# Kernel optimization log

Measured on AMD Instinct MI355X. Metric: run time of the kernel, lower is better.

The kernel has to match this reference:

```python
import jax, jax.numpy as jnp
import numpy as np

N, E, F_IN, C, H = 50000, 800000, 256, 64, 2  # nodes, edges, in-feat, per-head dim, heads
NEG_SLOPE_ATT = 0.2   # GATConv leaky_relu slope
NEG_SLOPE = 0.01      # F.leaky_relu default
BN_EPS = 1e-5


def setup_inputs() -> dict:
    key = jax.random.key(0)
    ks = jax.random.split(key, 10)
    x = jax.random.normal(ks[0], (N, F_IN), dtype=jnp.float32)
    edge_index = jax.random.randint(ks[1], (2, E), 0, N, dtype=jnp.int32)
    # GATConv params
    W = jax.random.normal(ks[2], (F_IN, H * C), dtype=jnp.float32) / np.sqrt(F_IN)
    att_src = jax.random.normal(ks[3], (H, C), dtype=jnp.float32) / np.sqrt(C)
    att_dst = jax.random.normal(ks[4], (H, C), dtype=jnp.float32) / np.sqrt(C)
    conv_bias = jnp.zeros((H * C,), dtype=jnp.float32)
    # fc1: in = hidden*2*2 = 256, out = hidden = 64
    fc1_w = jax.random.normal(ks[5], (H * C * 2, C), dtype=jnp.float32) / np.sqrt(H * C * 2)
    fc1_b = jnp.zeros((C,), dtype=jnp.float32)
    bn_gamma = jnp.ones((C,), dtype=jnp.float32)
    bn_beta = jnp.zeros((C,), dtype=jnp.float32)
    bn_mean = jnp.zeros((C,), dtype=jnp.float32)
    bn_var = jnp.ones((C,), dtype=jnp.float32)
    fc2_w = jax.random.normal(ks[6], (C, 3), dtype=jnp.float32) / np.sqrt(C)
    fc2_b = jnp.zeros((3,), dtype=jnp.float32)
    return {"x": x, "edge_index": edge_index, "W": W, "att_src": att_src,
            "att_dst": att_dst, "conv_bias": conv_bias, "fc1_w": fc1_w, "fc1_b": fc1_b,
            "bn_gamma": bn_gamma, "bn_beta": bn_beta, "bn_mean": bn_mean,
            "bn_var": bn_var, "fc2_w": fc2_w, "fc2_b": fc2_b}


def gat_conv(x, edge_index, W, att_src, att_dst, bias):
    # Project: [N, H, C]
    h = (x @ W).reshape(N, H, C)
    a_s = jnp.einsum('nhc,hc->nh', h, att_src)  # [N, H]
    a_d = jnp.einsum('nhc,hc->nh', h, att_dst)
    # add self-loops (PyG default)
    loops = jnp.arange(N, dtype=edge_index.dtype)
    src = jnp.concatenate([edge_index[0], loops])
    dst = jnp.concatenate([edge_index[1], loops])
    e = jax.nn.leaky_relu(a_s[src] + a_d[dst], NEG_SLOPE_ATT)  # [E+N, H]
    # segment softmax over incoming edges of each dst node
    m = jax.ops.segment_max(e, dst, num_segments=N)
    e_exp = jnp.exp(e - m[dst])
    denom = jax.ops.segment_sum(e_exp, dst, num_segments=N)
    alpha = e_exp / denom[dst]  # [E+N, H]
    msg = h[src] * alpha[:, :, None]  # [E+N, H, C]
    out = jax.ops.segment_sum(msg, dst, num_segments=N)  # [N, H, C]
    return out.reshape(N, H * C) + bias


def reference(x, edge_index, W, att_src, att_dst, conv_bias, fc1_w, fc1_b,
              bn_gamma, bn_beta, bn_mean, bn_var, fc2_w, fc2_b):
    # eval mode: dropout = identity, BN uses running stats
    h = gat_conv(x, edge_index, W, att_src, att_dst, conv_bias)
    h = jax.nn.leaky_relu(h, NEG_SLOPE)
    edge_rep = jnp.concatenate([h[edge_index[0]], h[edge_index[1]]], axis=1)  # [E, 256]
    y = edge_rep @ fc1_w + fc1_b
    y = (y - bn_mean) * jax.lax.rsqrt(bn_var + BN_EPS) * bn_gamma + bn_beta
    y = jax.nn.leaky_relu(y, NEG_SLOPE)
    return y @ fc2_w + fc2_b  # [E, 3]
```

## Files before the change

### kernel.cpp

```cpp
#include <hip/hip_runtime.h>
#include <hip/hip_bf16.h>

#define N_NODES 50000
#define N_EDGES 800000
#define F_IN    256
#define C_DIM   64
#define HC      128
#define NPG     6250
#define NBB     32
#define NBLK    196
#define XW_BLOCKS   3125
#define HIST_BLOCKS 256

typedef __attribute__((ext_vector_type(8))) short bf16x8;
typedef __attribute__((ext_vector_type(4))) float f32x4;

static constexpr size_t OFF_HBF   = 0;
static constexpr size_t OFF_AB    = 25600000;
static constexpr size_t OFF_AS    = 38400000;
static constexpr size_t OFF_AD    = 38800000;
static constexpr size_t OFF_OFFS  = 39200000;
static constexpr size_t OFF_TOT   = 39400064;
static constexpr size_t OFF_PART  = 39800064;
static constexpr size_t OFF_CSR2  = 39801088;
static constexpr size_t OFF_WT    = 46201088;
static constexpr size_t OFF_FC1T  = 46266624;
static constexpr size_t OFF_SCALE = 46299392;
static constexpr size_t OFF_CC    = 46299904;
static constexpr size_t OFF_FC2M  = 46300416;
static constexpr size_t OFF_BCNT  = 46302464;
static constexpr size_t OFF_BASE  = 52702464;

__device__ __forceinline__ float2 bf2(unsigned u) {
    float2 r;
    r.x = __uint_as_float(u << 16);
    r.y = __uint_as_float(u & 0xffff0000u);
    return r;
}
__device__ __forceinline__ unsigned short f2bf(float f) {
    unsigned u = __float_as_uint(f);
    return (unsigned short)((u + 0x7fffu + ((u >> 16) & 1u)) >> 16);
}
__device__ __forceinline__ short f2bf_s(float f) {
    __hip_bfloat16 h = __float2bfloat16(f);
    return *reinterpret_cast<short*>(&h);
}

__global__ __launch_bounds__(256) void k_prep(const float* __restrict__ W,
                                              const float* __restrict__ fc1,
                                              const float* __restrict__ fc1_b,
                                              const float* __restrict__ gamma,
                                              const float* __restrict__ beta,
                                              const float* __restrict__ mean,
                                              const float* __restrict__ var,
                                              const float* __restrict__ fc2_w,
                                              unsigned short* __restrict__ Wt,
                                              unsigned short* __restrict__ fc1t,
                                              float* __restrict__ scale,
                                              float* __restrict__ cc,
                                              unsigned short* __restrict__ fc2m) {
    int id = blockIdx.x * 256 + threadIdx.x;
    if (id < 32768) {
        int n = id >> 8, k = id & 255;
        Wt[id] = f2bf(W[k * HC + n]);
    }
    int id2 = id - 32768;
    if (id2 >= 0 && id2 < 16384) {
        int j = id2 >> 7, q = id2 & 127;
        int L = q >> 1, b = q & 1;
        int kch = 32 * (L >> 4) + (L & 15) + 16 * b;
        float v = (j < 64) ? fc1[kch * 64 + j] : fc1[(128 + kch) * 64 + (j - 64)];
        fc1t[id2] = f2bf(v);
    }
    int id3 = id - (32768 + 16384);
    if (id3 >= 0 && id3 < 128) {
        int jj = id3 & 63;
        float s = gamma[jj] * rsqrtf(var[jj] + 1e-5f);
        scale[id3] = s;
        cc[id3] = (id3 < 64) ? 0.f : (fc1_b[jj] - mean[jj]) * s + beta[jj];
    }
    int id4 = id - (32768 + 16384 + 128);
    if (id4 >= 0 && id4 < 1024) {
        int kk = id4 >> 9, rem = id4 & 511;
        int lane = rem >> 3, j = rem & 7;
        int q  = kk * 16 + (lane >> 4) * 4 + (j >> 1);
        int ch = 32 * (q >> 4) + (q & 15) + 16 * (j & 1);
        int col = lane & 15;
        float v = (col < 3) ? fc2_w[ch * 3 + col] : 0.f;
        fc2m[id4] = f2bf(v);
    }
}

__global__ __launch_bounds__(256, 4) void k_front(const float* __restrict__ x,
                                                  const unsigned short* __restrict__ Wt,
                                                  const float* __restrict__ att_src,
                                                  const float* __restrict__ att_dst,
                                                  unsigned* __restrict__ h_p,
                                                  float* __restrict__ as_,
                                                  float* __restrict__ ad_,
                                                  const int* __restrict__ dst,
                                                  int* __restrict__ bcnt) {
    __shared__ int smem[6464];
    const int t = threadIdx.x;

    if (blockIdx.x < HIST_BLOCKS) {
        int* hist = smem;
        const int bid = blockIdx.x;
        const int g  = bid & 7;
        const int bi = bid >> 3;
        const int lo = g * NPG, hi = lo + NPG;
        for (int j = t; j < NPG; j += 256) hist[j] = 0;
        __syncthreads();
        const int4* d4 = (const int4*)dst + bi * 6250;
#pragma unroll 1
        for (int it = 0; it < 25; ++it) {
            int idx = it * 256 + t;
            if (idx < 6250) {
                int4 d = d4[idx];
                if (d.x >= lo && d.x < hi) atomicAdd(&hist[d.x - lo], 1);
                if (d.y >= lo && d.y < hi) atomicAdd(&hist[d.y - lo], 1);
                if (d.z >= lo && d.z < hi) atomicAdd(&hist[d.z - lo], 1);
                if (d.w >= lo && d.w < hi) atomicAdd(&hist[d.w - lo], 1);
            }
        }
        __syncthreads();
        int* row = bcnt + (size_t)(g * NBB + bi) * NPG;
        for (int j = t; j < NPG; j += 256) row[j] = hist[j];
        return;
    }

    float* xs  = (float*)smem;
    float* sAs = (float*)(smem + 4096);
    float* sAd = sAs + 32;
    const int v    = t >> 6;
    const int lane = t & 63;
    const int c16  = lane & 15;
    const int kg   = lane >> 4;
    const int r0   = (blockIdx.x - HIST_BLOCKS) * 16;
    if (t < 32) { sAs[t] = 0.f; sAd[t] = 0.f; }
    {
        const float4* xsrc = (const float4*)(x + (size_t)r0 * F_IN);
        float4* xsl = (float4*)xs;
#pragma unroll
        for (int it = 0; it < 4; ++it) {
            int cidx = it * 256 + t;
            int rl = cidx >> 6, j = cidx & 63;
            float4 val = xsrc[cidx];
            xsl[rl * 64 + (j ^ rl)] = val;
        }
    }
    const int cf0 = 2 * v, cf1 = 2 * v + 1;
    bf16x8 wf0[8], wf1[8];
#pragma unroll
    for (int kk = 0; kk < 8; ++kk) {
        wf0[kk] = *(const bf16x8*)(Wt + (size_t)(cf0 * 16 + c16) * 256 + kk * 32 + kg * 8);
        wf1[kk] = *(const bf16x8*)(Wt + (size_t)(cf1 * 16 + c16) * 256 + kk * 32 + kg * 8);
    }
    __syncthreads();

    f32x4 acc0 = {}, acc1 = {};
#pragma unroll
    for (int kk = 0; kk < 8; ++kk) {
        int j0 = kk * 8 + kg * 2;
        float4 a0 = *(const float4*)(xs + (size_t)(c16 * 64 + (j0 ^ c16)) * 4);
        float4 a1 = *(const float4*)(xs + (size_t)(c16 * 64 + ((j0 + 1) ^ c16)) * 4);
        float fv[8] = {a0.x, a0.y, a0.z, a0.w, a1.x, a1.y, a1.z, a1.w};
        bf16x8 ahi, alo;
#pragma unroll
        for (int q = 0; q < 8; ++q) {
            unsigned u = __float_as_uint(fv[q]);
            float hval = __uint_as_float(u & 0xffff0000u);
            float d = fv[q] - hval;
            ahi[q] = (short)(u >> 16);
            alo[q] = (short)(__float_as_uint(d) >> 16);
        }
        acc0 = __builtin_amdgcn_mfma_f32_16x16x32_bf16(alo, wf0[kk], acc0, 0, 0, 0);
        acc0 = __builtin_amdgcn_mfma_f32_16x16x32_bf16(ahi, wf0[kk], acc0, 0, 0, 0);
        acc1 = __builtin_amdgcn_mfma_f32_16x16x32_bf16(alo, wf1[kk], acc1, 0, 0, 0);
        acc1 = __builtin_amdgcn_mfma_f32_16x16x32_bf16(ahi, wf1[kk], acc1, 0, 0, 0);
    }
#pragma unroll
    for (int i = 0; i < 4; ++i) {
        int row = r0 + kg * 4 + i;
        unsigned pu = (unsigned)f2bf(acc0[i]) | ((unsigned)f2bf(acc1[i]) << 16);
        h_p[(size_t)row * 64 + v * 16 + c16] = pu;
    }
    float ws0 = att_src[cf0 * 16 + c16], ws1 = att_src[cf1 * 16 + c16];
    float wd0 = att_dst[cf0 * 16 + c16], wd1 = att_dst[cf1 * 16 + c16];
    float pas[4], pad[4];
#pragma unroll
    for (int i = 0; i < 4; ++i) {
        pas[i] = acc0[i] * ws0 + acc1[i] * ws1;
        pad[i] = acc0[i] * wd0 + acc1[i] * wd1;
    }
#pragma unroll
    for (int m = 1; m < 16; m <<= 1) {
#pragma unroll
        for (int i = 0; i < 4; ++i) {
            pas[i] += __shfl_xor(pas[i], m, 64);
            pad[i] += __shfl_xor(pad[i], m, 64);
        }
    }
    const int head = v >> 1;
    if (c16 == 0) {
#pragma unroll
        for (int i = 0; i < 4; ++i) {
            atomicAdd(&sAs[(kg * 4 + i) * 2 + head], pas[i]);
            atomicAdd(&sAd[(kg * 4 + i) * 2 + head], pad[i]);
        }
    }
    __syncthreads();
    if (t < 32) {
        int row = t >> 1, hd = t & 1;
        as_[(r0 + row) * 2 + hd] = sAs[row * 2 + hd];
        ad_[(r0 + row) * 2 + hd] = sAd[row * 2 + hd];
    }
}

__global__ void k_tot_part(const int* __restrict__ bcnt, int* __restrict__ tot,
                           int* __restrict__ part) {
    __shared__ int sd[256];
    int n = blockIdx.x * 256 + threadIdx.x;
    int s = 0;
    if (n < N_NODES) {
        int g = n / NPG, ln = n - g * NPG;
        const int* col = bcnt + (size_t)g * NBB * NPG + ln;
#pragma unroll
        for (int bi = 0; bi < NBB; ++bi) s += col[bi * NPG];
        tot[n] = s;
    }
    sd[threadIdx.x] = s;
    __syncthreads();
    for (int off = 128; off > 0; off >>= 1) {
        if (threadIdx.x < off) sd[threadIdx.x] += sd[threadIdx.x + off];
        __syncthreads();
    }
    if (threadIdx.x == 0) part[blockIdx.x] = sd[0];
}

__global__ void k_scan_base(const int* __restrict__ tot, const int* __restrict__ part,
                            const int* __restrict__ bcnt, int* __restrict__ offs,
                            int* __restrict__ base) {
    __shared__ int sp[256];
    __shared__ int sd[256];
    const int t = threadIdx.x;
    int pv = (t < NBLK && t < (int)blockIdx.x) ? part[t] : 0;
    sp[t] = pv;
    __syncthreads();
    for (int off = 128; off > 0; off >>= 1) {
        if (t < off) sp[t] += sp[t + off];
        __syncthreads();
    }
    const int bb = sp[0];
    __syncthreads();
    int i = blockIdx.x * 256 + t;
    int v = (i < N_NODES) ? tot[i] : 0;
    sd[t] = v;
    __syncthreads();
    for (int off = 1; off < 256; off <<= 1) {
        int u = (t >= off) ? sd[t - off] : 0;
        __syncthreads();
        sd[t] += u;
        __syncthreads();
    }
    if (i < N_NODES) {
        int o = bb + sd[t] - v;
        offs[i] = o;
        if (i == N_NODES - 1) offs[N_NODES] = o + v;
        int g = i / NPG, ln = i - g * NPG;
        const int* col = bcnt + (size_t)g * NBB * NPG + ln;
        int* bcol = base + (size_t)g * NBB * NPG + ln;
        int run = o;
#pragma unroll
        for (int bi = 0; bi < NBB; ++bi) {
            bcol[bi * NPG] = run;
            run += col[bi * NPG];
        }
    }
}

__global__ __launch_bounds__(256) void k_scatter(const int* __restrict__ src,
                                                 const int* __restrict__ dst,
                                                 const int* __restrict__ base,
                                                 int2* __restrict__ csr2) {
    __shared__ int cnt[NPG];
    const int g  = blockIdx.x & 7;
    const int bi = blockIdx.x >> 3;
    const int lo = g * NPG, hi = lo + NPG;
    const int* brow = base + (size_t)(g * NBB + bi) * NPG;
    for (int j = threadIdx.x; j < NPG; j += 256) cnt[j] = brow[j];
    __syncthreads();
    const int4* d4 = (const int4*)dst + bi * 6250;
    const int4* s4 = (const int4*)src + bi * 6250;
    const int ebase = bi * 25000;
#pragma unroll 1
    for (int it = 0; it < 25; ++it) {
        int idx = it * 256 + threadIdx.x;
        if (idx < 6250) {
            int4 d = d4[idx];
            int4 s = s4[idx];
            int e = ebase + idx * 4;
            if (d.x >= lo && d.x < hi) { int p = atomicAdd(&cnt[d.x - lo], 1); csr2[p] = make_int2(s.x, e);     }
            if (d.y >= lo && d.y < hi) { int p = atomicAdd(&cnt[d.y - lo], 1); csr2[p] = make_int2(s.y, e + 1); }
            if (d.z >= lo && d.z < hi) { int p = atomicAdd(&cnt[d.z - lo], 1); csr2[p] = make_int2(s.z, e + 2); }
            if (d.w >= lo && d.w < hi) { int p = atomicAdd(&cnt[d.w - lo], 1); csr2[p] = make_int2(s.w, e + 3); }
        }
    }
}

__global__ __launch_bounds__(256) void k_agg_uv(const unsigned* __restrict__ h_p,
                                                const float* __restrict__ as_,
                                                const float* __restrict__ ad_,
                                                const int* __restrict__ offs,
                                                const int2* __restrict__ csr2,
                                                const float* __restrict__ conv_bias,
                                                const unsigned short* __restrict__ fc1t,
                                                const float* __restrict__ scale,
                                                const float* __restrict__ cc,
                                                unsigned* __restrict__ ab_p) {
    __shared__ unsigned lds_h2[16 * 68];
    const int t    = threadIdx.x;
    const int v    = t >> 6;
    const int lane = t & 63;
    const int ql   = lane & 15;
    const int q    = lane >> 4;
    const int hd   = ql >> 3;
    const int nbase = blockIdx.x * 16;
    const uint4* h4 = (const uint4*)h_p;

#pragma unroll 1
    for (int j = 0; j < 4; ++j) {
        const int ln = v * 4 + j;
        const int n  = nbase + ln;
        const float adn = ad_[n * 2 + hd];
        float a[8] = {};
        float accw = 0.f;
        const int beg = offs[n], end = offs[n + 1];
        int i = beg + q;
        for (; i + 4 < end; i += 8) {
            int s0 = csr2[i].x;
            int s1 = csr2[i + 4].x;
            uint4 u0 = h4[(unsigned)(s0 * 16 + ql)];
            uint4 u1 = h4[(unsigned)(s1 * 16 + ql)];
            float l0 = as_[s0 * 2 + hd] + adn;
            float l1 = as_[s1 * 2 + hd] + adn;
            l0 = fmaxf(l0, 0.2f * l0);
            l1 = fmaxf(l1, 0.2f * l1);
            float w0 = __expf(l0), w1 = __expf(l1);
            float2 tt;
            tt = bf2(u0.x); a[0] += w0 * tt.x; a[1] += w0 * tt.y;
            tt = bf2(u0.y); a[2] += w0 * tt.x; a[3] += w0 * tt.y;
            tt = bf2(u0.z); a[4] += w0 * tt.x; a[5] += w0 * tt.y;
            tt = bf2(u0.w); a[6] += w0 * tt.x; a[7] += w0 * tt.y;
            tt = bf2(u1.x); a[0] += w1 * tt.x; a[1] += w1 * tt.y;
            tt = bf2(u1.y); a[2] += w1 * tt.x; a[3] += w1 * tt.y;
            tt = bf2(u1.z); a[4] += w1 * tt.x; a[5] += w1 * tt.y;
            tt = bf2(u1.w); a[6] += w1 * tt.x; a[7] += w1 * tt.y;
            accw += w0 + w1;
        }
        if (i < end) {
            int s0 = csr2[i].x;
            uint4 u0 = h4[(unsigned)(s0 * 16 + ql)];
            float l0 = as_[s0 * 2 + hd] + adn;
            l0 = fmaxf(l0, 0.2f * l0);
            float w0 = __expf(l0);
            float2 tt;
            tt = bf2(u0.x); a[0] += w0 * tt.x; a[1] += w0 * tt.y;
            tt = bf2(u0.y); a[2] += w0 * tt.x; a[3] += w0 * tt.y;
            tt = bf2(u0.z); a[4] += w0 * tt.x; a[5] += w0 * tt.y;
            tt = bf2(u0.w); a[6] += w0 * tt.x; a[7] += w0 * tt.y;
            accw += w0;
        }
#pragma unroll
        for (int m = 16; m < 64; m <<= 1) {
#pragma unroll
            for (int jj = 0; jj < 8; ++jj) a[jj] += __shfl_xor(a[jj], m, 64);
            accw += __shfl_xor(accw, m, 64);
        }
        if (q == 0) {
            float es = as_[n * 2 + hd] + adn;
            es = fmaxf(es, 0.2f * es);
            float wsl = __expf(es);
            uint4 un = h4[(unsigned)(n * 16 + ql)];
            float2 tt;
            tt = bf2(un.x); a[0] += wsl * tt.x; a[1] += wsl * tt.y;
            tt = bf2(un.y); a[2] += wsl * tt.x; a[3] += wsl * tt.y;
            tt = bf2(un.z); a[4] += wsl * tt.x; a[5] += wsl * tt.y;
            tt = bf2(un.w); a[6] += wsl * tt.x; a[7] += wsl * tt.y;
            accw += wsl;
            float rinv = 1.f / accw;
            unsigned pw[4];
#pragma unroll
            for (int jj = 0; jj < 4; ++jj) {
                int w = 4 * ql + jj;
                int c = 32 * (w >> 4) + (w & 15);
                float o0 = a[2 * jj] * rinv + conv_bias[c];
                float o1 = a[2 * jj + 1] * rinv + conv_bias[c + 16];
                o0 = fmaxf(o0, 0.01f * o0);
                o1 = fmaxf(o1, 0.01f * o1);
                pw[jj] = (unsigned)f2bf(o0) | ((unsigned)f2bf(o1) << 16);
            }
            *(uint4*)&lds_h2[ln * 68 + ql * 4] = make_uint4(pw[0], pw[1], pw[2], pw[3]);
        }
    }
    __syncthreads();

    const int c16 = lane & 15;
    const int kg  = lane >> 4;
    const int cf0 = 2 * v, cf1 = 2 * v + 1;
    bf16x8 af[4];
#pragma unroll
    for (int kk = 0; kk < 4; ++kk)
        af[kk] = *(const bf16x8*)&lds_h2[c16 * 68 + kk * 16 + kg * 4];
    f32x4 acc0 = {}, acc1 = {};
#pragma unroll
    for (int kk = 0; kk < 4; ++kk) {
        bf16x8 b0 = *(const bf16x8*)(fc1t + (size_t)(cf0 * 16 + c16) * HC + kk * 32 + kg * 8);
        bf16x8 b1 = *(const bf16x8*)(fc1t + (size_t)(cf1 * 16 + c16) * HC + kk * 32 + kg * 8);
        acc0 = __builtin_amdgcn_mfma_f32_16x16x32_bf16(af[kk], b0, acc0, 0, 0, 0);
        acc1 = __builtin_amdgcn_mfma_f32_16x16x32_bf16(af[kk], b1, acc1, 0, 0, 0);
    }
    const int j0 = cf0 * 16 + c16, j1 = j0 + 16;
    const float s0 = scale[j0], s1 = scale[j1];
    const float q0 = cc[j0],    q1 = cc[j1];
#pragma unroll
    for (int i = 0; i < 4; ++i) {
        int row = nbase + kg * 4 + i;
        unsigned pu = (unsigned)f2bf(acc0[i] * s0 + q0)
                    | ((unsigned)f2bf(acc1[i] * s1 + q1) << 16);
        ab_p[(size_t)row * 64 + v * 16 + c16] = pu;
    }
}

__device__ __forceinline__ void mk_afrag(uint4 ua, const float* bb, bf16x8& ap) {
    float2 t; float z;
    t = bf2(ua.x);
    z = t.x + bb[0]; z = fmaxf(z, 0.01f * z); ap[0] = f2bf_s(z);
    z = t.y + bb[1]; z = fmaxf(z, 0.01f * z); ap[1] = f2bf_s(z);
    t = bf2(ua.y);
    z = t.x + bb[2]; z = fmaxf(z, 0.01f * z); ap[2] = f2bf_s(z);
    z = t.y + bb[3]; z = fmaxf(z, 0.01f * z); ap[3] = f2bf_s(z);
    t = bf2(ua.z);
    z = t.x + bb[4]; z = fmaxf(z, 0.01f * z); ap[4] = f2bf_s(z);
    z = t.y + bb[5]; z = fmaxf(z, 0.01f * z); ap[5] = f2bf_s(z);
    t = bf2(ua.w);
    z = t.x + bb[6]; z = fmaxf(z, 0.01f * z); ap[6] = f2bf_s(z);
    z = t.y + bb[7]; z = fmaxf(z, 0.01f * z); ap[7] = f2bf_s(z);
}

__global__ __launch_bounds__(256) void k_edge(const int* __restrict__ offs,
                                              const int2* __restrict__ csr2,
                                              const unsigned* __restrict__ ab_p,
                                              const unsigned short* __restrict__ fc2m,
                                              const float* __restrict__ fc2_b,
                                              float* __restrict__ out) {
    const int n    = blockIdx.x * 4 + (threadIdx.x >> 6);
    const int lane = threadIdx.x & 63;
    const int c16  = lane & 15;
    const int kg   = lane >> 4;
    bf16x8 bfr0 = *(const bf16x8*)(fc2m + (size_t)lane * 8);
    bf16x8 bfr1 = *(const bf16x8*)(fc2m + (size_t)(64 + lane) * 8);
    const uint4* abv = (const uint4*)ab_p;
    uint4 ub0 = abv[(unsigned)(n * 16 + 8 + kg)];
    uint4 ub1 = abv[(unsigned)(n * 16 + 12 + kg)];
    float bb0[8], bb1[8];
    {
        float2 t;
        t = bf2(ub0.x); bb0[0] = t.x; bb0[1] = t.y;
        t = bf2(ub0.y); bb0[2] = t.x; bb0[3] = t.y;
        t = bf2(ub0.z); bb0[4] = t.x; bb0[5] = t.y;
        t = bf2(ub0.w); bb0[6] = t.x; bb0[7] = t.y;
        t = bf2(ub1.x); bb1[0] = t.x; bb1[1] = t.y;
        t = bf2(ub1.y); bb1[2] = t.x; bb1[3] = t.y;
        t = bf2(ub1.z); bb1[4] = t.x; bb1[5] = t.y;
        t = bf2(ub1.w); bb1[6] = t.x; bb1[7] = t.y;
    }
    const float ob = (c16 < 3) ? fc2_b[c16] : 0.f;
    const int beg = offs[n], end = offs[n + 1];
    for (int base = beg; base < end; base += 16) {
        int slot = base + c16;
        int2 ce = (slot < end) ? csr2[slot] : make_int2(0, 0);
        uint4 ua0 = abv[(unsigned)(ce.x * 16 + kg)];
        uint4 ua1 = abv[(unsigned)(ce.x * 16 + 4 + kg)];
        bf16x8 ap0, ap1;
        mk_afrag(ua0, bb0, ap0);
        mk_afrag(ua1, bb1, ap1);
        f32x4 acc = {};
        acc = __builtin_amdgcn_mfma_f32_16x16x32_bf16(ap0, bfr0, acc, 0, 0, 0);
        acc = __builtin_amdgcn_mfma_f32_16x16x32_bf16(ap1, bfr1, acc, 0, 0, 0);
#pragma unroll
        for (int i = 0; i < 4; ++i) {
            int eid = __shfl(ce.y, kg * 4 + i, 64);
            if (c16 < 3 && (base + kg * 4 + i) < end)
                out[(size_t)eid * 3 + c16] = acc[i] + ob;
        }
    }
}

extern "C" void kernel_launch(void* const* d_in, const int* in_sizes, int n_in,
                              void* d_out, int out_size, void* d_ws, size_t ws_size,
                              hipStream_t stream) {
    const float* x        = (const float*)d_in[0];
    const int*   ei       = (const int*)d_in[1];
    const float* W        = (const float*)d_in[2];
    const float* att_src  = (const float*)d_in[3];
    const float* att_dst  = (const float*)d_in[4];
    const float* conv_b   = (const float*)d_in[5];
    const float* fc1_w    = (const float*)d_in[6];
    const float* fc1_b    = (const float*)d_in[7];
    const float* gamma    = (const float*)d_in[8];
    const float* beta     = (const float*)d_in[9];
    const float* mean     = (const float*)d_in[10];
    const float* var      = (const float*)d_in[11];
    const float* fc2_w    = (const float*)d_in[12];
    const float* fc2_b    = (const float*)d_in[13];
    float*       out      = (float*)d_out;
    char*        ws       = (char*)d_ws;

    const int* src = ei;
    const int* dst = ei + N_EDGES;

    unsigned*       h_p   = (unsigned*)(ws + OFF_HBF);
    unsigned*       ab_p  = (unsigned*)(ws + OFF_AB);
    float*          as_   = (float*)(ws + OFF_AS);
    float*          ad_   = (float*)(ws + OFF_AD);
    int*            offs  = (int*)(ws + OFF_OFFS);
    int*            tot   = (int*)(ws + OFF_TOT);
    int*            part  = (int*)(ws + OFF_PART);
    int2*           csr2  = (int2*)(ws + OFF_CSR2);
    unsigned short* Wt    = (unsigned short*)(ws + OFF_WT);
    unsigned short* fc1t  = (unsigned short*)(ws + OFF_FC1T);
    float*          scale = (float*)(ws + OFF_SCALE);
    float*          cc    = (float*)(ws + OFF_CC);
    unsigned short* fc2m  = (unsigned short*)(ws + OFF_FC2M);
    int*            bcnt  = (int*)(ws + OFF_BCNT);
    int*            base  = (int*)(ws + OFF_BASE);

    k_prep<<<235, 256, 0, stream>>>(W, fc1_w, fc1_b, gamma, beta, mean, var, fc2_w,
                                    Wt, fc1t, scale, cc, fc2m);

    k_front<<<HIST_BLOCKS + XW_BLOCKS, 256, 0, stream>>>(x, Wt, att_src, att_dst,
                                                         h_p, as_, ad_, dst, bcnt);

    k_tot_part <<<NBLK, 256, 0, stream>>>(bcnt, tot, part);
    k_scan_base<<<NBLK, 256, 0, stream>>>(tot, part, bcnt, offs, base);
    k_scatter  <<<8 * NBB, 256, 0, stream>>>(src, dst, base, csr2);

    k_agg_uv<<<N_NODES / 16, 256, 0, stream>>>(h_p, as_, ad_, offs, csr2, conv_b,
                                               fc1t, scale, cc, ab_p);
    k_edge  <<<N_NODES / 4, 256, 0, stream>>>(offs, csr2, ab_p, fc2m, fc2_b, out);
}
```

Baseline: 151.6 us.

## Process edges in original order in edge kernel and shrink CSR to source-only

The edge MLP kernel now walks edges in their original order, one 16-edge tile per wave, instead of walking each destination node's CSR segment. Each tile gathers both the source and destination precomputed halves, and its output rows are written contiguously rather than scattered through stored edge ids. The CSR therefore only needs source indices, which halves the scatter writes and the aggregation reads. The cost is an extra random gather of the destination half per edge (previously loaded once per node). It also removes per-node loop imbalance and partially empty tiles.

```diff
diff --git a/kernel.cpp b/kernel.cpp
--- a/kernel.cpp
+++ b/kernel.cpp
@@ -22,7 +22,7 @@
 static constexpr size_t OFF_OFFS  = 39200000;
 static constexpr size_t OFF_TOT   = 39400064;
 static constexpr size_t OFF_PART  = 39800064;
-static constexpr size_t OFF_CSR2  = 39801088;
+static constexpr size_t OFF_CSR   = 39801088;
 static constexpr size_t OFF_WT    = 46201088;
 static constexpr size_t OFF_FC1T  = 46266624;
 static constexpr size_t OFF_SCALE = 46299392;
@@ -282,7 +282,7 @@
 __global__ __launch_bounds__(256) void k_scatter(const int* __restrict__ src,
                                                  const int* __restrict__ dst,
                                                  const int* __restrict__ base,
-                                                 int2* __restrict__ csr2) {
+                                                 int* __restrict__ csr) {
     __shared__ int cnt[NPG];
     const int g  = blockIdx.x & 7;
     const int bi = blockIdx.x >> 3;
@@ -292,18 +292,16 @@
     __syncthreads();
     const int4* d4 = (const int4*)dst + bi * 6250;
     const int4* s4 = (const int4*)src + bi * 6250;
-    const int ebase = bi * 25000;
 #pragma unroll 1
     for (int it = 0; it < 25; ++it) {
         int idx = it * 256 + threadIdx.x;
         if (idx < 6250) {
             int4 d = d4[idx];
             int4 s = s4[idx];
-            int e = ebase + idx * 4;
-            if (d.x >= lo && d.x < hi) { int p = atomicAdd(&cnt[d.x - lo], 1); csr2[p] = make_int2(s.x, e);     }
-            if (d.y >= lo && d.y < hi) { int p = atomicAdd(&cnt[d.y - lo], 1); csr2[p] = make_int2(s.y, e + 1); }
-            if (d.z >= lo && d.z < hi) { int p = atomicAdd(&cnt[d.z - lo], 1); csr2[p] = make_int2(s.z, e + 2); }
-            if (d.w >= lo && d.w < hi) { int p = atomicAdd(&cnt[d.w - lo], 1); csr2[p] = make_int2(s.w, e + 3); }
+            if (d.x >= lo && d.x < hi) { int p = atomicAdd(&cnt[d.x - lo], 1); csr[p] = s.x; }
+            if (d.y >= lo && d.y < hi) { int p = atomicAdd(&cnt[d.y - lo], 1); csr[p] = s.y; }
+            if (d.z >= lo && d.z < hi) { int p = atomicAdd(&cnt[d.z - lo], 1); csr[p] = s.z; }
+            if (d.w >= lo && d.w < hi) { int p = atomicAdd(&cnt[d.w - lo], 1); csr[p] = s.w; }
         }
     }
 }
@@ -312,7 +310,7 @@
                                                 const float* __restrict__ as_,
                                                 const float* __restrict__ ad_,
                                                 const int* __restrict__ offs,
-                                                const int2* __restrict__ csr2,
+                                                const int* __restrict__ csr,
                                                 const float* __restrict__ conv_bias,
                                                 const unsigned short* __restrict__ fc1t,
                                                 const float* __restrict__ scale,
@@ -338,8 +336,8 @@
         const int beg = offs[n], end = offs[n + 1];
         int i = beg + q;
         for (; i + 4 < end; i += 8) {
-            int s0 = csr2[i].x;
-            int s1 = csr2[i + 4].x;
+            int s0 = csr[i];
+            int s1 = csr[i + 4];
             uint4 u0 = h4[(unsigned)(s0 * 16 + ql)];
             uint4 u1 = h4[(unsigned)(s1 * 16 + ql)];
             float l0 = as_[s0 * 2 + hd] + adn;
@@ -359,7 +357,7 @@
             accw += w0 + w1;
         }
         if (i < end) {
-            int s0 = csr2[i].x;
+            int s0 = csr[i];
             uint4 u0 = h4[(unsigned)(s0 * 16 + ql)];
             float l0 = as_[s0 * 2 + hd] + adn;
             l0 = fmaxf(l0, 0.2f * l0);
@@ -432,68 +430,53 @@
     }
 }
 
-__device__ __forceinline__ void mk_afrag(uint4 ua, const float* bb, bf16x8& ap) {
-    float2 t; float z;
-    t = bf2(ua.x);
-    z = t.x + bb[0]; z = fmaxf(z, 0.01f * z); ap[0] = f2bf_s(z);
-    z = t.y + bb[1]; z = fmaxf(z, 0.01f * z); ap[1] = f2bf_s(z);
-    t = bf2(ua.y);
-    z = t.x + bb[2]; z = fmaxf(z, 0.01f * z); ap[2] = f2bf_s(z);
-    z = t.y + bb[3]; z = fmaxf(z, 0.01f * z); ap[3] = f2bf_s(z);
-    t = bf2(ua.z);
-    z = t.x + bb[4]; z = fmaxf(z, 0.01f * z); ap[4] = f2bf_s(z);
-    z = t.y + bb[5]; z = fmaxf(z, 0.01f * z); ap[5] = f2bf_s(z);
-    t = bf2(ua.w);
-    z = t.x + bb[6]; z = fmaxf(z, 0.01f * z); ap[6] = f2bf_s(z);
-    z = t.y + bb[7]; z = fmaxf(z, 0.01f * z); ap[7] = f2bf_s(z);
-}
-
-__global__ __launch_bounds__(256) void k_edge(const int* __restrict__ offs,
-                                              const int2* __restrict__ csr2,
+__device__ __forceinline__ void mk_afrag2(uint4 ua, uint4 ub, bf16x8& ap) {
+    float2 a, b; float z;
+    a = bf2(ua.x); b = bf2(ub.x);
+    z = a.x + b.x; z = fmaxf(z, 0.01f * z); ap[0] = f2bf_s(z);
+    z = a.y + b.y; z = fmaxf(z, 0.01f * z); ap[1] = f2bf_s(z);
+    a = bf2(ua.y); b = bf2(ub.y);
+    z = a.x + b.x; z = fmaxf(z, 0.01f * z); ap[2] = f2bf_s(z);
+    z = a.y + b.y; z = fmaxf(z, 0.01f * z); ap[3] = f2bf_s(z);
+    a = bf2(ua.z); b = bf2(ub.z);
+    z = a.x + b.x; z = fmaxf(z, 0.01f * z); ap[4] = f2bf_s(z);
+    z = a.y + b.y; z = fmaxf(z, 0.01f * z); ap[5] = f2bf_s(z);
+    a = bf2(ua.w); b = bf2(ub.w);
+    z = a.x + b.x; z = fmaxf(z, 0.01f * z); ap[6] = f2bf_s(z);
+    z = a.y + b.y; z = fmaxf(z, 0.01f * z); ap[7] = f2bf_s(z);
+}
+
+__global__ __launch_bounds__(256) void k_edge(const int* __restrict__ src,
+                                              const int* __restrict__ dst,
                                               const unsigned* __restrict__ ab_p,
                                               const unsigned short* __restrict__ fc2m,
                                               const float* __restrict__ fc2_b,
                                               float* __restrict__ out) {
-    const int n    = blockIdx.x * 4 + (threadIdx.x >> 6);
+    const int wid  = blockIdx.x * 4 + (threadIdx.x >> 6);
     const int lane = threadIdx.x & 63;
     const int c16  = lane & 15;
     const int kg   = lane >> 4;
+    const int e0   = wid * 16;
+    const int e    = e0 + c16;
     bf16x8 bfr0 = *(const bf16x8*)(fc2m + (size_t)lane * 8);
     bf16x8 bfr1 = *(const bf16x8*)(fc2m + (size_t)(64 + lane) * 8);
     const uint4* abv = (const uint4*)ab_p;
-    uint4 ub0 = abv[(unsigned)(n * 16 + 8 + kg)];
-    uint4 ub1 = abv[(unsigned)(n * 16 + 12 + kg)];
-    float bb0[8], bb1[8];
-    {
-        float2 t;
-        t = bf2(ub0.x); bb0[0] = t.x; bb0[1] = t.y;
-        t = bf2(ub0.y); bb0[2] = t.x; bb0[3] = t.y;
-        t = bf2(ub0.z); bb0[4] = t.x; bb0[5] = t.y;
-        t = bf2(ub0.w); bb0[6] = t.x; bb0[7] = t.y;
-        t = bf2(ub1.x); bb1[0] = t.x; bb1[1] = t.y;
-        t = bf2(ub1.y); bb1[2] = t.x; bb1[3] = t.y;
-        t = bf2(ub1.z); bb1[4] = t.x; bb1[5] = t.y;
-        t = bf2(ub1.w); bb1[6] = t.x; bb1[7] = t.y;
-    }
-    const float ob = (c16 < 3) ? fc2_b[c16] : 0.f;
-    const int beg = offs[n], end = offs[n + 1];
-    for (int base = beg; base < end; base += 16) {
-        int slot = base + c16;
-        int2 ce = (slot < end) ? csr2[slot] : make_int2(0, 0);
-        uint4 ua0 = abv[(unsigned)(ce.x * 16 + kg)];
-        uint4 ua1 = abv[(unsigned)(ce.x * 16 + 4 + kg)];
-        bf16x8 ap0, ap1;
-        mk_afrag(ua0, bb0, ap0);
-        mk_afrag(ua1, bb1, ap1);
-        f32x4 acc = {};
-        acc = __builtin_amdgcn_mfma_f32_16x16x32_bf16(ap0, bfr0, acc, 0, 0, 0);
-        acc = __builtin_amdgcn_mfma_f32_16x16x32_bf16(ap1, bfr1, acc, 0, 0, 0);
-#pragma unroll
-        for (int i = 0; i < 4; ++i) {
-            int eid = __shfl(ce.y, kg * 4 + i, 64);
-            if (c16 < 3 && (base + kg * 4 + i) < end)
-                out[(size_t)eid * 3 + c16] = acc[i] + ob;
-        }
+    const int s = src[e], d = dst[e];
+    uint4 ua0 = abv[(unsigned)(s * 16 + kg)];
+    uint4 ua1 = abv[(unsigned)(s * 16 + 4 + kg)];
+    uint4 ub0 = abv[(unsigned)(d * 16 + 8 + kg)];
+    uint4 ub1 = abv[(unsigned)(d * 16 + 12 + kg)];
+    bf16x8 ap0, ap1;
+    mk_afrag2(ua0, ub0, ap0);
+    mk_afrag2(ua1, ub1, ap1);
+    f32x4 acc = {};
+    acc = __builtin_amdgcn_mfma_f32_16x16x32_bf16(ap0, bfr0, acc, 0, 0, 0);
+    acc = __builtin_amdgcn_mfma_f32_16x16x32_bf16(ap1, bfr1, acc, 0, 0, 0);
+    if (c16 < 3) {
+        const float ob = fc2_b[c16];
+#pragma unroll
+        for (int i = 0; i < 4; ++i)
+            out[(size_t)(e0 + kg * 4 + i) * 3 + c16] = acc[i] + ob;
     }
 }
 
@@ -527,7 +510,7 @@
     int*            offs  = (int*)(ws + OFF_OFFS);
     int*            tot   = (int*)(ws + OFF_TOT);
     int*            part  = (int*)(ws + OFF_PART);
-    int2*           csr2  = (int2*)(ws + OFF_CSR2);
+    int*            csr   = (int*)(ws + OFF_CSR);
     unsigned short* Wt    = (unsigned short*)(ws + OFF_WT);
     unsigned short* fc1t  = (unsigned short*)(ws + OFF_FC1T);
     float*          scale = (float*)(ws + OFF_SCALE);
@@ -544,9 +527,9 @@
 
     k_tot_part <<<NBLK, 256, 0, stream>>>(bcnt, tot, part);
     k_scan_base<<<NBLK, 256, 0, stream>>>(tot, part, bcnt, offs, base);
-    k_scatter  <<<8 * NBB, 256, 0, stream>>>(src, dst, base, csr2);
-
-    k_agg_uv<<<N_NODES / 16, 256, 0, stream>>>(h_p, as_, ad_, offs, csr2, conv_b,
+    k_scatter  <<<8 * NBB, 256, 0, stream>>>(src, dst, base, csr);
+
+    k_agg_uv<<<N_NODES / 16, 256, 0, stream>>>(h_p, as_, ad_, offs, csr, conv_b,
                                                fc1t, scale, cc, ab_p);
-    k_edge  <<<N_NODES / 4, 256, 0, stream>>>(offs, csr2, ab_p, fc2m, fc2_b, out);
-}
+    k_edge  <<<N_EDGES / 64, 256, 0, stream>>>(src, dst, ab_p, fc2m, fc2_b, out);
+}
```

Result: no change. 150.6 us (-0.6%).
